# Kernel tuning notes

Measured on AMD Instinct MI355X. Metric: run time of the kernel, lower is better.

Reference implementation:

```python
import jax, jax.numpy as jnp
import numpy as np

EMBED = 256; HEADS = 8; LEVELS = 4; POINTS = 4; DIM = EMBED // HEADS


def _bilinear_gather(vflat, H, W, px, py):
    """grid_sample(mode='bilinear', padding='zeros', align_corners=False).
    vflat: (bs, heads, H*W, d); px, py: (bs, heads, nq, P) pixel coords.
    Returns (bs, heads, nq, P, d).
    """
    x0 = jnp.floor(px); y0 = jnp.floor(py)
    x1 = x0 + 1.0;      y1 = y0 + 1.0
    wx1 = px - x0; wx0 = 1.0 - wx1
    wy1 = py - y0; wy0 = 1.0 - wy1

    def corner(ix, iy, w):
        valid = (ix >= 0) & (ix <= W - 1) & (iy >= 0) & (iy <= H - 1)
        idx = (jnp.clip(iy, 0, H - 1) * W + jnp.clip(ix, 0, W - 1)).astype(jnp.int32)
        b, h, nq, P = idx.shape
        g = jnp.take_along_axis(vflat, idx.reshape(b, h, nq * P)[..., None], axis=2)
        g = g.reshape(b, h, nq, P, -1)
        return g * (w * valid)[..., None]

    return (corner(x0, y0, wx0 * wy0) + corner(x1, y0, wx1 * wy0)
            + corner(x0, y1, wx0 * wy1) + corner(x1, y1, wx1 * wy1))


def _ms_deform_attn(value4, shapes, loc, attn):
    """value4 (bs,nv,heads,D); loc (bs,nq,heads,L,P,2) in [0,1];
    attn (bs,nq,heads,L,P). Returns (bs,nq,heads*D)."""
    bs, nq = loc.shape[0], loc.shape[1]
    grids = 2.0 * loc - 1.0
    attn_t = jnp.transpose(attn, (0, 2, 1, 3, 4))  # (bs,heads,nq,L,P)
    out = jnp.zeros((bs, HEADS, nq, DIM), value4.dtype)
    start = 0
    for lvl in range(LEVELS):
        H, W = int(shapes[lvl, 0]), int(shapes[lvl, 1])
        v = value4[:, start:start + H * W]                 # (bs,HW,heads,D)
        vflat = jnp.transpose(v, (0, 2, 1, 3))             # (bs,heads,HW,D)
        g = jnp.transpose(grids[:, :, :, lvl], (0, 2, 1, 3, 4))  # (bs,heads,nq,P,2)
        px = (g[..., 0] + 1.0) * (W * 0.5) - 0.5
        py = (g[..., 1] + 1.0) * (H * 0.5) - 0.5
        sampled = _bilinear_gather(vflat, H, W, px, py)    # (bs,heads,nq,P,D)
        out = out + jnp.einsum('bhqpd,bhqp->bhqd', sampled, attn_t[:, :, :, lvl])
        start += H * W
    return jnp.transpose(out, (0, 2, 1, 3)).reshape(bs, nq, HEADS * DIM)


def _forward(query, value, query_pos, reference_points, last_reference_offsets,
             shapes, Wv, bv, Wo, bo, Wa, ba, Wout, bout):
    identity = query
    q = query + query_pos
    bs, nq, _ = q.shape
    nv = value.shape[1]
    v = (value @ Wv + bv).reshape(bs, nv, HEADS, DIM)
    off = (q @ Wo + bo).reshape(bs, nq, HEADS, LEVELS, POINTS, 2)
    attn = jax.nn.softmax((q @ Wa + ba).reshape(bs, nq, HEADS, LEVELS * POINTS), axis=-1)
    attn = attn.reshape(bs, nq, HEADS, LEVELS, POINTS)
    wh = jnp.asarray(np.asarray(shapes)[:, ::-1].copy(), jnp.float32)  # (L,2) as (w,h)
    loc = (reference_points[:, :, None, :, None, :]
           + off / wh[None, None, None, :, None, :]
           + last_reference_offsets[:, :, :, None, None, :])  # flow-guided per-head shift
    out = _ms_deform_attn(v, shapes, loc, attn)
    return out @ Wout + bout + identity  # dropout is identity at eval


def setup_inputs() -> dict:
    key = jax.random.key(0)
    ks = jax.random.split(key, 10)
    bs, nq = 8, 1200
    shapes = np.array([[92, 160], [46, 80], [23, 40], [12, 20]], np.int64)
    nv = int((shapes[:, 0] * shapes[:, 1]).sum())
    f = jnp.float32
    return {
        "query": jax.random.normal(ks[0], (bs, nq, EMBED), f),
        "value": jax.random.normal(ks[1], (bs, nv, EMBED), f),
        "query_pos": jax.random.normal(ks[2], (bs, nq, EMBED), f),
        "reference_points": jax.random.uniform(ks[3], (bs, nq, LEVELS, 2), f),
        "last_reference_offsets": jax.random.normal(ks[4], (bs, nq, HEADS, 2), f) * 0.02,
        "spatial_shapes": shapes,
        "Wv": jax.random.normal(ks[5], (EMBED, EMBED), f) * 0.02,
        "bv": jnp.zeros((EMBED,), f),
        "Wo": jax.random.normal(ks[6], (EMBED, HEADS * LEVELS * POINTS * 2), f) * 0.02,
        "bo": jax.random.normal(ks[7], (HEADS * LEVELS * POINTS * 2,), f) * 0.02,
        "Wa": jax.random.normal(ks[8], (EMBED, HEADS * LEVELS * POINTS), f) * 0.02,
        "ba": jnp.zeros((HEADS * LEVELS * POINTS,), f),
        "Wout": jax.random.normal(ks[9], (EMBED, EMBED), f) * 0.02,
        "bout": jnp.zeros((EMBED,), f),
    }


def reference(query, value, query_pos, reference_points, last_reference_offsets,
              spatial_shapes, Wv, bv, Wo, bo, Wa, ba, Wout, bout):
    return _forward(query, value, query_pos, reference_points, last_reference_offsets,
                    spatial_shapes, Wv, bv, Wo, bo, Wa, ba, Wout, bout)
```

## Files before the change

### kernel.cpp

```cpp
#include <hip/hip_runtime.h>
#include <math.h>

#define BS 8
#define NQ 1200
#define NV 19560
#define EMB 256

typedef __bf16 bf16;
typedef bf16 bf16x8 __attribute__((ext_vector_type(8)));
typedef float f32x4 __attribute__((ext_vector_type(4)));
typedef float f32x16 __attribute__((ext_vector_type(16)));

static __device__ __forceinline__ bf16x8 cvt8(float4 a, float4 b) {
    bf16x8 r;
    r[0] = (bf16)a.x; r[1] = (bf16)a.y; r[2] = (bf16)a.z; r[3] = (bf16)a.w;
    r[4] = (bf16)b.x; r[5] = (bf16)b.y; r[6] = (bf16)b.z; r[7] = (bf16)b.w;
    return r;
}

static __device__ __forceinline__ void gl16(const void* g, void* l) {
    __builtin_amdgcn_global_load_lds(
        (const __attribute__((address_space(1))) void*)g,
        (__attribute__((address_space(3))) void*)l, 16, 0, 0);
}

__global__ __launch_bounds__(256) void prep_k(
    const float* __restrict__ Wv, const float* __restrict__ Wo,
    const float* __restrict__ Wa, const float* __restrict__ Wout,
    const float* __restrict__ query, const float* __restrict__ qpos,
    bf16* __restrict__ Wv_p, bf16* __restrict__ Wo_p,
    bf16* __restrict__ Wa_p, bf16* __restrict__ Wout_p, bf16* __restrict__ qsum)
{
    int bid = blockIdx.x, tid = threadIdx.x;
    if (bid < 896) {
        const float* src; bf16* dst; int N, t0;
        if (bid < 256)      { src = Wv;   dst = Wv_p;   N = 256; t0 = bid * 256; }
        else if (bid < 512) { src = Wo;   dst = Wo_p;   N = 256; t0 = (bid - 256) * 256; }
        else if (bid < 640) { src = Wa;   dst = Wa_p;   N = 128; t0 = (bid - 512) * 256; }
        else                { src = Wout; dst = Wout_p; N = 256; t0 = (bid - 640) * 256; }
        int t = t0 + tid;
        int n = t >> 8, k = t & 255;
        dst[t] = (bf16)src[k * N + n];
    } else {
        int t = (bid - 896) * 256 + tid;
        qsum[t] = (bf16)(query[t] + qpos[t]);
    }
}

__global__ __launch_bounds__(256, 1) void vgemm_k(
    const float* __restrict__ A, const bf16* __restrict__ Bp,
    const float* __restrict__ bias, bf16* __restrict__ outB, int Mtiles)
{
    __shared__ __align__(16) bf16  sB[256 * 256];
    __shared__ __align__(16) float sA[4 * 2 * 1024];
    const int tid = threadIdx.x;
    const int lane = tid & 63;
    const int w = tid >> 6;
    const int l16 = lane & 15;
    const int qd = lane >> 4;

#pragma unroll
    for (int i = 0; i < 32; ++i) {
        int s = i * 256 + tid;
        int r = s >> 5, p = s & 31, c = p ^ (r & 7);
        gl16(Bp + (size_t)r * 256 + c * 8, sB + ((size_t)i * 256 + w * 64) * 8);
    }

    float* sAw = sA + w * 2048;
    const int lr4 = lane >> 4, sl = lane & 15;
    int aoff[4];
#pragma unroll
    for (int i = 0; i < 4; ++i) {
        int lr = i * 4 + lr4;
        aoff[i] = (w * 16 + lr) * 256 + ((sl ^ (lr & 7)) * 4);
    }
    auto stageA = [&](int t, int kc, int buf) {
        const float* base = A + (size_t)t * 16384 + kc * 64;
#pragma unroll
        for (int i = 0; i < 4; ++i)
            gl16(base + aoff[i], sAw + buf * 1024 + i * 256);
    };

    int t = blockIdx.x;
    stageA(t, 0, 0);
    stageA(t, 1, 1);

    float bb[16];
#pragma unroll
    for (int ct = 0; ct < 16; ++ct) bb[ct] = bias[ct * 16 + l16];

    __syncthreads();

    const int akey = l16 & 7;
    f32x4 acc[16];

    auto compute = [&](int kc, int buf) {
        const float* ar = sAw + buf * 1024 + l16 * 64;
#pragma unroll
        for (int ks = 0; ks < 2; ++ks) {
            int kg = kc * 2 + ks;
            int s  = ks * 8 + qd * 2;
            float4 a0 = *(const float4*)(ar + ((s    ) ^ akey) * 4);
            float4 a1 = *(const float4*)(ar + ((s + 1) ^ akey) * 4);
            bf16x8 af = cvt8(a0, a1);
#pragma unroll
            for (int ct = 0; ct < 16; ++ct) {
                int brow = ct * 16 + l16;
                bf16x8 bfr = *(const bf16x8*)(sB + (size_t)brow * 256 +
                                              ((kg * 4 + qd) ^ (brow & 7)) * 8);
                acc[ct] = __builtin_amdgcn_mfma_f32_16x16x32_bf16(af, bfr, acc[ct], 0, 0, 0);
            }
        }
    };

#define VM_WAIT4 asm volatile("s_waitcnt vmcnt(4)" ::: "memory")
#define VM_WAIT0 asm volatile("s_waitcnt vmcnt(0)" ::: "memory")

    while (true) {
#pragma unroll
        for (int ct = 0; ct < 16; ++ct) acc[ct] = (f32x4){0.f, 0.f, 0.f, 0.f};

        VM_WAIT4; compute(0, 0); stageA(t, 2, 0);
        VM_WAIT4; compute(1, 1); stageA(t, 3, 1);
        VM_WAIT4; compute(2, 0);
        VM_WAIT0; compute(3, 1);

#pragma unroll
        for (int ct = 0; ct < 16; ++ct) {
            int col = ct * 16 + l16;
#pragma unroll
            for (int r = 0; r < 4; ++r) {
                int row = t * 64 + w * 16 + qd * 4 + r;
                outB[(size_t)row * 256 + col] = (bf16)(acc[ct][r] + bb[ct]);
            }
        }

        int tn = t + gridDim.x;
        if (tn >= Mtiles) break;
        stageA(tn, 0, 0);
        stageA(tn, 1, 1);
        t = tn;
    }
#undef VM_WAIT4
#undef VM_WAIT0
}

template <int NS, int NB, bool HAS_RES, bool OUT_BF16>
__global__ __launch_bounds__(256, 2) void gemm3_k(
    const bf16* __restrict__ Ah, const bf16* __restrict__ Bp,
    const float* __restrict__ bias, const float* __restrict__ res,
    float* __restrict__ outF, bf16* __restrict__ outB, int Mtiles)
{
    constexpr int CT = NB / 16;
    __shared__ __align__(16) bf16 sB[NB * 256];
    const int tid = threadIdx.x;
    const int lane = tid & 63;
    const int w = tid >> 6;
    const int l16 = lane & 15;
    const int qd = lane >> 4;
    const int col0 = (blockIdx.x & 1) * NB;
    const int tstride = gridDim.x >> 1;
    const bf16* Bsrc = Bp + (size_t)col0 * 256;

    uint4 curH[8], nxtH[8];
    auto loadA = [&](int t, uint4* dH) {
        size_t rb = ((size_t)t * 64 + w * 16 + l16) * 256;
#pragma unroll
        for (int kc = 0; kc < 8; ++kc)
            dH[kc] = *(const uint4*)(Ah + rb + kc * 32 + qd * 8);
    };

    int tile = blockIdx.x >> 1;
    if (tile < Mtiles) loadA(tile, curH);

#pragma unroll
    for (int i = 0; i < NB * 32 / 256; ++i) {
        int s = i * 256 + tid;
        int r = s >> 5, p = s & 31, c = p ^ (r & 7);
        gl16(Bsrc + (size_t)r * 256 + c * 8, sB + (size_t)(i * 256 + w * 64) * 8);
    }
    __syncthreads();

    for (; tile < Mtiles; tile += tstride) {
        int nt = tile + tstride;
        if (nt < Mtiles) loadA(nt, nxtH);

        f32x4 acc[CT];
#pragma unroll
        for (int c = 0; c < CT; ++c) acc[c] = (f32x4){0.f, 0.f, 0.f, 0.f};
#pragma unroll
        for (int kc = 0; kc < 8; ++kc) {
            bf16x8 af = *(const bf16x8*)&curH[kc];
#pragma unroll
            for (int ct = 0; ct < CT; ++ct) {
                int brow = ct * 16 + l16;
                int chunk = (kc * 4 + qd) ^ (l16 & 7);
                bf16x8 bfr = *(const bf16x8*)(sB + (size_t)brow * 256 + chunk * 8);
                acc[ct] = __builtin_amdgcn_mfma_f32_16x16x32_bf16(af, bfr, acc[ct], 0, 0, 0);
            }
        }
#pragma unroll
        for (int ct = 0; ct < CT; ++ct) {
            int col = col0 + ct * 16 + l16;
            float bbv = bias[col];
#pragma unroll
            for (int r = 0; r < 4; ++r) {
                int row = tile * 64 + w * 16 + qd * 4 + r;
                size_t idx = (size_t)row * NS + col;
                float v = acc[ct][r] + bbv;
                if (HAS_RES) v += res[idx];
                if (OUT_BF16) outB[idx] = (bf16)v;
                else          outF[idx] = v;
            }
        }
#pragma unroll
        for (int i = 0; i < 8; ++i) curH[i] = nxtH[i];
    }
}

static __device__ __forceinline__ void b8f(uint4 u, float* f) {
    f[0] = __uint_as_float(u.x << 16); f[1] = __uint_as_float(u.x & 0xffff0000u);
    f[2] = __uint_as_float(u.y << 16); f[3] = __uint_as_float(u.y & 0xffff0000u);
    f[4] = __uint_as_float(u.z << 16); f[5] = __uint_as_float(u.z & 0xffff0000u);
    f[6] = __uint_as_float(u.w << 16); f[7] = __uint_as_float(u.w & 0xffff0000u);
}

__global__ __launch_bounds__(256) void sample4_k(
    const bf16* __restrict__ vv, const float* __restrict__ offb,
    const float* __restrict__ attnb, const float* __restrict__ refp,
    const float* __restrict__ lref, bf16* __restrict__ outb)
{
    const int cH[4] = {92, 46, 23, 12};
    const int cW[4] = {160, 80, 40, 20};
    const int cS[4] = {0, 14720, 18400, 19320};
    const int w = threadIdx.x >> 6;
    const int lane = threadIdx.x & 63;
    const int wid = blockIdx.x * 4 + w;
    const int bq = wid >> 3, h = wid & 7;
    const int b = bq / NQ;
    const int p = lane >> 2, dg = lane & 3;
    const int lvl = p >> 2;

    float logit = attnb[(size_t)bq * 128 + h * 16 + p];
    float mx = logit;
#pragma unroll
    for (int s = 4; s < 64; s <<= 1) mx = fmaxf(mx, __shfl_xor(mx, s));
    float e = __expf(logit - mx);
    float ssum = e;
#pragma unroll
    for (int s = 4; s < 64; s <<= 1) ssum += __shfl_xor(ssum, s);
    float wgt = e / ssum;

    const int Hh = cH[lvl], Ww = cW[lvl];
    float ox = offb[(size_t)bq * 256 + h * 32 + p * 2];
    float oy = offb[(size_t)bq * 256 + h * 32 + p * 2 + 1];
    float rx = refp[(size_t)bq * 8 + lvl * 2];
    float ry = refp[(size_t)bq * 8 + lvl * 2 + 1];
    float lrx = lref[(size_t)bq * 16 + h * 2];
    float lry = lref[(size_t)bq * 16 + h * 2 + 1];

    float px = (rx + ox / (float)Ww + lrx) * (float)Ww - 0.5f;
    float py = (ry + oy / (float)Hh + lry) * (float)Hh - 0.5f;
    float x0f = floorf(px), y0f = floorf(py);
    int x0 = (int)x0f, y0 = (int)y0f;
    float wx1 = px - x0f, wx0 = 1.f - wx1;
    float wy1 = py - y0f, wy0 = 1.f - wy1;
    bool xa = (unsigned)x0 < (unsigned)Ww, xb = (unsigned)(x0 + 1) < (unsigned)Ww;
    bool ya = (unsigned)y0 < (unsigned)Hh, yb = (unsigned)(y0 + 1) < (unsigned)Hh;
    int xc0 = min(max(x0, 0), Ww - 1), xc1 = min(max(x0 + 1, 0), Ww - 1);
    int yc0 = min(max(y0, 0), Hh - 1), yc1 = min(max(y0 + 1, 0), Hh - 1);
    float w00 = wgt * wx0 * wy0 * (float)(xa && ya);
    float w01 = wgt * wx1 * wy0 * (float)(xb && ya);
    float w10 = wgt * wx0 * wy1 * (float)(xa && yb);
    float w11 = wgt * wx1 * wy1 * (float)(xb && yb);

    const bf16* vb = vv + ((size_t)b * NV + cS[lvl]) * 256 + h * 32 + dg * 8;
    uint4 g00 = *(const uint4*)(vb + ((size_t)yc0 * Ww + xc0) * 256);
    uint4 g01 = *(const uint4*)(vb + ((size_t)yc0 * Ww + xc1) * 256);
    uint4 g10 = *(const uint4*)(vb + ((size_t)yc1 * Ww + xc0) * 256);
    uint4 g11 = *(const uint4*)(vb + ((size_t)yc1 * Ww + xc1) * 256);

    float acc[8], f[8];
    b8f(g00, f);
#pragma unroll
    for (int j = 0; j < 8; j++) acc[j] = w00 * f[j];
    b8f(g01, f);
#pragma unroll
    for (int j = 0; j < 8; j++) acc[j] = fmaf(w01, f[j], acc[j]);
    b8f(g10, f);
#pragma unroll
    for (int j = 0; j < 8; j++) acc[j] = fmaf(w10, f[j], acc[j]);
    b8f(g11, f);
#pragma unroll
    for (int j = 0; j < 8; j++) acc[j] = fmaf(w11, f[j], acc[j]);

#pragma unroll
    for (int s = 4; s < 64; s <<= 1)
#pragma unroll
        for (int j = 0; j < 8; j++) acc[j] += __shfl_xor(acc[j], s);

    if (p == 0) {
        bf16x8 o;
#pragma unroll
        for (int j = 0; j < 8; j++) o[j] = (bf16)acc[j];
        *(bf16x8*)(outb + (size_t)bq * 256 + h * 32 + dg * 8) = o;
    }
}

extern "C" void kernel_launch(void* const* d_in, const int* in_sizes, int n_in,
                              void* d_out, int out_size, void* d_ws, size_t ws_size,
                              hipStream_t stream) {
    (void)in_sizes; (void)n_in; (void)out_size; (void)ws_size;
    const float* query = (const float*)d_in[0];
    const float* value = (const float*)d_in[1];
    const float* qpos  = (const float*)d_in[2];
    const float* refp  = (const float*)d_in[3];
    const float* lref  = (const float*)d_in[4];
    const float* Wv   = (const float*)d_in[6];
    const float* bv   = (const float*)d_in[7];
    const float* Wo   = (const float*)d_in[8];
    const float* bo   = (const float*)d_in[9];
    const float* Wa   = (const float*)d_in[10];
    const float* ba   = (const float*)d_in[11];
    const float* Wout = (const float*)d_in[12];
    const float* bout = (const float*)d_in[13];

    char* ws = (char*)d_ws;
    bf16*  Wv_p   = (bf16*)(ws + 0);
    bf16*  Wo_p   = (bf16*)(ws + 131072);
    bf16*  Wa_p   = (bf16*)(ws + 262144);
    bf16*  Wout_p = (bf16*)(ws + 327680);
    bf16*  qsum   = (bf16*)(ws + 458752);
    float* off_b  = (float*)(ws + 5373952);
    float* attn_b = (float*)(ws + 15204352);
    bf16*  tsa_b  = (bf16*)(ws + 20119552);
    bf16*  v_b    = (bf16*)(ws + 25034752);

    prep_k<<<10496, 256, 0, stream>>>(Wv, Wo, Wa, Wout, query, qpos,
                                      Wv_p, Wo_p, Wa_p, Wout_p, qsum);

    vgemm_k<<<256, 256, 0, stream>>>(value, Wv_p, bv, v_b, (BS * NV) / 64);
    gemm3_k<256, 128, false, false><<<300, 256, 0, stream>>>(
        qsum, Wo_p, bo, nullptr, off_b, nullptr, (BS * NQ) / 64);
    gemm3_k<128, 64, false, false><<<300, 256, 0, stream>>>(
        qsum, Wa_p, ba, nullptr, attn_b, nullptr, (BS * NQ) / 64);
    sample4_k<<<(BS * NQ * 8) / 4, 256, 0, stream>>>(v_b, off_b, attn_b, refp, lref, tsa_b);
    gemm3_k<256, 128, true, false><<<300, 256, 0, stream>>>(
        tsa_b, Wout_p, bout, query, (float*)d_out, nullptr, (BS * NQ) / 64);
}
```

Baseline: 392.4 us.

## Store value projection head-major and fuse offset/attention GEMMs into one launch

```diff
diff --git a/kernel.cpp b/kernel.cpp
--- a/kernel.cpp
+++ b/kernel.cpp
@@ -5,6 +5,7 @@
 #define NQ 1200
 #define NV 19560
 #define EMB 256
+#define TPB 306
 
 typedef __bf16 bf16;
 typedef bf16 bf16x8 __attribute__((ext_vector_type(8)));
@@ -28,8 +29,10 @@
     const float* __restrict__ Wv, const float* __restrict__ Wo,
     const float* __restrict__ Wa, const float* __restrict__ Wout,
     const float* __restrict__ query, const float* __restrict__ qpos,
+    const float* __restrict__ bo, const float* __restrict__ ba,
     bf16* __restrict__ Wv_p, bf16* __restrict__ Wo_p,
-    bf16* __restrict__ Wa_p, bf16* __restrict__ Wout_p, bf16* __restrict__ qsum)
+    bf16* __restrict__ Wa_p, bf16* __restrict__ Wout_p,
+    bf16* __restrict__ qsum, float* __restrict__ cb)
 {
     int bid = blockIdx.x, tid = threadIdx.x;
     if (bid < 896) {
@@ -41,9 +44,12 @@
         int t = t0 + tid;
         int n = t >> 8, k = t & 255;
         dst[t] = (bf16)src[k * N + n];
-    } else {
+    } else if (bid < 10496) {
         int t = (bid - 896) * 256 + tid;
         qsum[t] = (bf16)(query[t] + qpos[t]);
+    } else {
+        cb[tid] = bo[tid];
+        if (tid < 128) cb[256 + tid] = ba[tid];
     }
 }
 
@@ -68,22 +74,26 @@
 
     float* sAw = sA + w * 2048;
     const int lr4 = lane >> 4, sl = lane & 15;
-    int aoff[4];
+    int swz4[4];
 #pragma unroll
     for (int i = 0; i < 4; ++i) {
         int lr = i * 4 + lr4;
-        aoff[i] = (w * 16 + lr) * 256 + ((sl ^ (lr & 7)) * 4);
-    }
-    auto stageA = [&](int t, int kc, int buf) {
-        const float* base = A + (size_t)t * 16384 + kc * 64;
-#pragma unroll
-        for (int i = 0; i < 4; ++i)
-            gl16(base + aoff[i], sAw + buf * 1024 + i * 256);
+        swz4[i] = (sl ^ (lr & 7)) * 4;
+    }
+    auto stageT = [&](int b_, int p0_, int kc, int buf) {
+#pragma unroll
+        for (int i = 0; i < 4; ++i) {
+            int pix = p0_ + w * 16 + i * 4 + lr4;
+            pix = min(pix, NV - 1);
+            gl16(A + ((size_t)b_ * NV + pix) * 256 + swz4[i] + kc * 64,
+                 sAw + buf * 1024 + i * 256);
+        }
     };
 
     int t = blockIdx.x;
-    stageA(t, 0, 0);
-    stageA(t, 1, 1);
+    int b = t / TPB, p0 = (t - b * TPB) * 64;
+    stageT(b, p0, 0, 0);
+    stageT(b, p0, 1, 1);
 
     float bb[16];
 #pragma unroll
@@ -120,32 +130,34 @@
 #pragma unroll
         for (int ct = 0; ct < 16; ++ct) acc[ct] = (f32x4){0.f, 0.f, 0.f, 0.f};
 
-        VM_WAIT4; compute(0, 0); stageA(t, 2, 0);
-        VM_WAIT4; compute(1, 1); stageA(t, 3, 1);
+        VM_WAIT4; compute(0, 0); stageT(b, p0, 2, 0);
+        VM_WAIT4; compute(1, 1); stageT(b, p0, 3, 1);
         VM_WAIT4; compute(2, 0);
         VM_WAIT0; compute(3, 1);
 
 #pragma unroll
         for (int ct = 0; ct < 16; ++ct) {
-            int col = ct * 16 + l16;
+            const bf16* dst0 = outB + ((size_t)(b * 8 + (ct >> 1)) * NV) * 32 + (ct & 1) * 16 + l16;
 #pragma unroll
             for (int r = 0; r < 4; ++r) {
-                int row = t * 64 + w * 16 + qd * 4 + r;
-                outB[(size_t)row * 256 + col] = (bf16)(acc[ct][r] + bb[ct]);
+                int pix = p0 + w * 16 + qd * 4 + r;
+                if (pix < NV)
+                    *(bf16*)(dst0 + (size_t)pix * 32) = (bf16)(acc[ct][r] + bb[ct]);
             }
         }
 
         int tn = t + gridDim.x;
         if (tn >= Mtiles) break;
-        stageA(tn, 0, 0);
-        stageA(tn, 1, 1);
         t = tn;
+        b = t / TPB; p0 = (t - b * TPB) * 64;
+        stageT(b, p0, 0, 0);
+        stageT(b, p0, 1, 1);
     }
 #undef VM_WAIT4
 #undef VM_WAIT0
 }
 
-template <int NS, int NB, bool HAS_RES, bool OUT_BF16>
+template <int NS, int NB, int NGRP, bool HAS_RES, bool OUT_BF16>
 __global__ __launch_bounds__(256, 2) void gemm3_k(
     const bf16* __restrict__ Ah, const bf16* __restrict__ Bp,
     const float* __restrict__ bias, const float* __restrict__ res,
@@ -158,8 +170,8 @@
     const int w = tid >> 6;
     const int l16 = lane & 15;
     const int qd = lane >> 4;
-    const int col0 = (blockIdx.x & 1) * NB;
-    const int tstride = gridDim.x >> 1;
+    const int col0 = (blockIdx.x % NGRP) * NB;
+    const int tstride = gridDim.x / NGRP;
     const bf16* Bsrc = Bp + (size_t)col0 * 256;
 
     uint4 curH[8], nxtH[8];
@@ -170,7 +182,7 @@
             dH[kc] = *(const uint4*)(Ah + rb + kc * 32 + qd * 8);
     };
 
-    int tile = blockIdx.x >> 1;
+    int tile = blockIdx.x / NGRP;
     if (tile < Mtiles) loadA(tile, curH);
 
 #pragma unroll
@@ -208,7 +220,7 @@
                 int row = tile * 64 + w * 16 + qd * 4 + r;
                 size_t idx = (size_t)row * NS + col;
                 float v = acc[ct][r] + bbv;
-                if (HAS_RES) v += res[idx];
+                if (HAS_RES) v += res[(size_t)row * 256 + col];
                 if (OUT_BF16) outB[idx] = (bf16)v;
                 else          outF[idx] = v;
             }
@@ -226,9 +238,9 @@
 }
 
 __global__ __launch_bounds__(256) void sample4_k(
-    const bf16* __restrict__ vv, const float* __restrict__ offb,
-    const float* __restrict__ attnb, const float* __restrict__ refp,
-    const float* __restrict__ lref, bf16* __restrict__ outb)
+    const bf16* __restrict__ vv, const float* __restrict__ comb,
+    const float* __restrict__ refp, const float* __restrict__ lref,
+    bf16* __restrict__ outb)
 {
     const int cH[4] = {92, 46, 23, 12};
     const int cW[4] = {160, 80, 40, 20};
@@ -241,7 +253,7 @@
     const int p = lane >> 2, dg = lane & 3;
     const int lvl = p >> 2;
 
-    float logit = attnb[(size_t)bq * 128 + h * 16 + p];
+    float logit = comb[(size_t)bq * 384 + 256 + h * 16 + p];
     float mx = logit;
 #pragma unroll
     for (int s = 4; s < 64; s <<= 1) mx = fmaxf(mx, __shfl_xor(mx, s));
@@ -252,8 +264,8 @@
     float wgt = e / ssum;
 
     const int Hh = cH[lvl], Ww = cW[lvl];
-    float ox = offb[(size_t)bq * 256 + h * 32 + p * 2];
-    float oy = offb[(size_t)bq * 256 + h * 32 + p * 2 + 1];
+    float ox = comb[(size_t)bq * 384 + h * 32 + p * 2];
+    float oy = comb[(size_t)bq * 384 + h * 32 + p * 2 + 1];
     float rx = refp[(size_t)bq * 8 + lvl * 2];
     float ry = refp[(size_t)bq * 8 + lvl * 2 + 1];
     float lrx = lref[(size_t)bq * 16 + h * 2];
@@ -274,11 +286,11 @@
     float w10 = wgt * wx0 * wy1 * (float)(xa && yb);
     float w11 = wgt * wx1 * wy1 * (float)(xb && yb);
 
-    const bf16* vb = vv + ((size_t)b * NV + cS[lvl]) * 256 + h * 32 + dg * 8;
-    uint4 g00 = *(const uint4*)(vb + ((size_t)yc0 * Ww + xc0) * 256);
-    uint4 g01 = *(const uint4*)(vb + ((size_t)yc0 * Ww + xc1) * 256);
-    uint4 g10 = *(const uint4*)(vb + ((size_t)yc1 * Ww + xc0) * 256);
-    uint4 g11 = *(const uint4*)(vb + ((size_t)yc1 * Ww + xc1) * 256);
+    const bf16* vb = vv + ((size_t)(b * 8 + h) * NV + cS[lvl]) * 32 + dg * 8;
+    uint4 g00 = *(const uint4*)(vb + ((size_t)yc0 * Ww + xc0) * 32);
+    uint4 g01 = *(const uint4*)(vb + ((size_t)yc0 * Ww + xc1) * 32);
+    uint4 g10 = *(const uint4*)(vb + ((size_t)yc1 * Ww + xc0) * 32);
+    uint4 g11 = *(const uint4*)(vb + ((size_t)yc1 * Ww + xc1) * 32);
 
     float acc[8], f[8];
     b8f(g00, f);
@@ -331,20 +343,18 @@
     bf16*  Wa_p   = (bf16*)(ws + 262144);
     bf16*  Wout_p = (bf16*)(ws + 327680);
     bf16*  qsum   = (bf16*)(ws + 458752);
-    float* off_b  = (float*)(ws + 5373952);
-    float* attn_b = (float*)(ws + 15204352);
+    float* comb   = (float*)(ws + 5373952);
     bf16*  tsa_b  = (bf16*)(ws + 20119552);
     bf16*  v_b    = (bf16*)(ws + 25034752);
-
-    prep_k<<<10496, 256, 0, stream>>>(Wv, Wo, Wa, Wout, query, qpos,
-                                      Wv_p, Wo_p, Wa_p, Wout_p, qsum);
-
-    vgemm_k<<<256, 256, 0, stream>>>(value, Wv_p, bv, v_b, (BS * NV) / 64);
-    gemm3_k<256, 128, false, false><<<300, 256, 0, stream>>>(
-        qsum, Wo_p, bo, nullptr, off_b, nullptr, (BS * NQ) / 64);
-    gemm3_k<128, 64, false, false><<<300, 256, 0, stream>>>(
-        qsum, Wa_p, ba, nullptr, attn_b, nullptr, (BS * NQ) / 64);
-    sample4_k<<<(BS * NQ * 8) / 4, 256, 0, stream>>>(v_b, off_b, attn_b, refp, lref, tsa_b);
-    gemm3_k<256, 128, true, false><<<300, 256, 0, stream>>>(
+    float* cbias  = (float*)(ws + 105152512);
+
+    prep_k<<<10497, 256, 0, stream>>>(Wv, Wo, Wa, Wout, query, qpos, bo, ba,
+                                      Wv_p, Wo_p, Wa_p, Wout_p, qsum, cbias);
+
+    vgemm_k<<<256, 256, 0, stream>>>(value, Wv_p, bv, v_b, BS * TPB);
+    gemm3_k<384, 128, 3, false, false><<<450, 256, 0, stream>>>(
+        qsum, Wo_p, cbias, nullptr, comb, nullptr, (BS * NQ) / 64);
+    sample4_k<<<(BS * NQ * 8) / 4, 256, 0, stream>>>(v_b, comb, refp, lref, tsa_b);
+    gemm3_k<256, 128, 2, true, false><<<300, 256, 0, stream>>>(
         tsa_b, Wout_p, bout, query, (float*)d_out, nullptr, (BS * NQ) / 64);
 }
```

Measured after the change: 395.8 us. About the same (+0.9%).
